# Kernel optimization log

Measured on AMD Instinct MI355X. Metric: run time of the kernel, lower is better.

The kernel has to match this reference:

```python
import jax, jax.numpy as jnp
import numpy as np

WS = 8          # window_size
WSU = 2 * WS    # window_size_up
HEADS = 8
SHIFT = WS // 2


def _build_idx(nH, nW):
    # Faithful reproduction of the torch window-reordering index (static numpy).
    if nH % 2 == 0:
        idx_H = np.arange(nH).reshape(2, -1).transpose(1, 0).reshape(-1)
    else:
        idx_H = np.arange(nH + 1).reshape(2, -1).transpose(1, 0).reshape(-1)[:-1]
    if nW % 2 == 0:
        idx_W = np.arange(nW).reshape(2, -1).transpose(1, 0).reshape(-1)
    else:
        idx_W = np.arange(nW + 1).reshape(2, -1).transpose(1, 0).reshape(-1)[:-1]
    idx = np.array([list(idx_W + i * nW) for i in range(nW)])
    return np.asarray(idx[list(idx_H)].reshape(-1))


def _rel_pos_index():
    # coords over the query window offset by ws//2; reference coords over the 2ws x 2ws KV window
    ch = np.arange(WS // 2, WS + WS // 2)
    cw = np.arange(WS // 2, WS + WS // 2)
    coords = np.stack(np.meshgrid(ch, cw, indexing='ij')).reshape(2, -1)        # (2, 64)
    rh = np.arange(2 * WS)
    rw = np.arange(2 * WS)
    ref = np.stack(np.meshgrid(rh, rw, indexing='ij')).reshape(2, -1)           # (2, 256)
    rel = coords[:, :, None] - ref[:, None, :]                                  # (2, 64, 256)
    rel = rel.transpose(1, 2, 0).copy()
    rel[..., 0] += 2 * WS - 1
    rel[..., 1] += 2 * WS - 1
    rel[..., 0] *= 4 * WS - 1
    return rel.sum(-1)  # (64, 256)


def setup_inputs() -> dict:
    key = jax.random.key(0)
    ks = jax.random.split(key, 4)
    C = 256
    return {
        'x': jax.random.normal(ks[0], (8, 128, 128, C), dtype=jnp.float32),
        'mask': jnp.zeros((1, 1, 1), dtype=jnp.float32),  # unused by the module's forward
        'qkv_w': jax.random.normal(ks[1], (3 * C, C), dtype=jnp.float32) * 0.02,
        'qkv_b': jnp.zeros((3 * C,), dtype=jnp.float32),
        'proj_w': jax.random.normal(ks[2], (C, C), dtype=jnp.float32) * 0.02,
        'proj_b': jnp.zeros((C,), dtype=jnp.float32),
        'rel_table': jax.random.normal(ks[3], ((4 * WS - 1) * (4 * WS - 1), HEADS), dtype=jnp.float32) * 0.02,
    }


def reference(x, mask, qkv_w, qkv_b, proj_w, proj_b, rel_table):
    B, H, W, C = x.shape
    hd = C // HEADS
    scale = hd ** (-0.5)

    pad_b = (WS - H % WS) % WS
    pad_r = (WS - W % WS) % WS
    x = jnp.pad(x, ((0, 0), (0, pad_b), (0, pad_r), (0, 0)))
    Hp, Wp = H + pad_b, W + pad_r

    qkv = (x @ qkv_w.T + qkv_b).reshape(B, Hp, Wp, 3, C)
    q = qkv[..., 0, :]                                    # (B, Hp, Wp, C)
    kv = jnp.moveaxis(qkv[..., 1:, :], 3, 0)              # (2, B, Hp, Wp, C)

    # pad KV for cross-window context
    kv = jnp.pad(kv, ((0, 0), (0, 0), (SHIFT, WS - SHIFT), (SHIFT, WS - SHIFT), (0, 0)))
    Hpkv, Wpkv = Hp + WS, Wp + WS

    nH, nW = Hp // WS, Wp // WS
    nHs, nWs = Hpkv // WSU, Wpkv // WSU
    nHsh, nWsh = nH - nHs, nW - nWs

    kv1 = kv[:, :, :nHs * WSU, :nWs * WSU]
    kv2 = kv[:, :, :nHs * WSU, WS:WS + nWsh * WSU]
    kv3 = kv[:, :, WS:WS + nHsh * WSU, :nWs * WSU]
    kv4 = kv[:, :, WS:WS + nHsh * WSU, WS:WS + nWsh * WSU]
    cross = jnp.concatenate([jnp.concatenate([kv1, kv2], axis=3),
                             jnp.concatenate([kv3, kv4], axis=3)], axis=2)

    # window partition at WSU -> (2, B, nH*nW, WSU*WSU, C), then reorder windows
    cross = cross.reshape(2, B, nH, WSU, nW, WSU, C).transpose(0, 1, 2, 4, 3, 5, 6)
    cross = cross.reshape(2, B, nH * nW, WSU * WSU, C)
    cross = cross[:, :, _build_idx(nH, nW)]

    Bw = B * nH * nW
    M = WSU * WSU  # 4*WS*WS KV tokens per window
    N = WS * WS    # query tokens per window
    k = cross[0].reshape(Bw, M, HEADS, hd)
    v = cross[1].reshape(Bw, M, HEADS, hd)

    qw = q.reshape(B, nH, WS, nW, WS, C).transpose(0, 1, 3, 2, 4, 5).reshape(Bw, N, HEADS, hd)

    attn = jnp.einsum('bnhd,bmhd->bhnm', qw * scale, k)   # (Bw, HEADS, N, M)
    bias = rel_table[_rel_pos_index()]                    # (N, M, HEADS)
    attn = jax.nn.softmax(attn + bias.transpose(2, 0, 1)[None], axis=-1)

    out = jnp.einsum('bhnm,bmhd->bnhd', attn, v).reshape(Bw, N, C)
    out = out @ proj_w.T + proj_b

    out = out.reshape(B, nH, nW, WS, WS, C).transpose(0, 1, 3, 2, 4, 5).reshape(B, Hp, Wp, C)
    return out[:, :H, :W, :].reshape(B, H * W, C)
```

## Files before the change

kernel.cpp:

```cpp
#include <hip/hip_runtime.h>
#include <hip/hip_bf16.h>
#include <stdint.h>

typedef __bf16 bf16;
typedef __bf16 bf16x4 __attribute__((ext_vector_type(4)));
typedef __bf16 bf16x8 __attribute__((ext_vector_type(8)));
typedef float f32x4 __attribute__((ext_vector_type(4)));

#define MFMA_BF16(a, b, c) __builtin_amdgcn_mfma_f32_16x16x32_bf16((a), (b), (c), 0, 0, 0)

#define LOG2E 1.4426950408889634f
#define QSCALE (0.17677669529663687f * 1.4426950408889634f)

__device__ __forceinline__ void load16f(const float* p, float* r) {
#pragma unroll
  for (int i = 0; i < 4; ++i) {
    float4 v = *(const float4*)(p + 4 * i);
    r[4 * i + 0] = v.x; r[4 * i + 1] = v.y; r[4 * i + 2] = v.z; r[4 * i + 3] = v.w;
  }
}

__device__ __forceinline__ void store16_bf16(bf16* dst, const float* r) {
  bf16x8 v0, v1;
#pragma unroll
  for (int i = 0; i < 8; ++i) { v0[i] = (bf16)r[i]; v1[i] = (bf16)r[8 + i]; }
  *(bf16x8*)(dst) = v0;
  *(bf16x8*)(dst + 8) = v1;
}

__global__ __launch_bounds__(256)
void cvt_bf16(const float* __restrict__ X, const float* __restrict__ Wq,
              bf16* __restrict__ Xb, bf16* __restrict__ Wqb)
{
  const unsigned t = blockIdx.x * 256 + threadIdx.x;
  const float* src;
  bf16* dst;
  if (t < 4194304u) { src = X + (size_t)t * 8; dst = Xb + (size_t)t * 8; }
  else {
    const unsigned u = t - 4194304u;
    src = Wq + (size_t)u * 8; dst = Wqb + (size_t)u * 8;
  }
  const float4 a = ((const float4*)src)[0];
  const float4 b = ((const float4*)src)[1];
  bf16x8 v;
  v[0] = (bf16)a.x; v[1] = (bf16)a.y; v[2] = (bf16)a.z; v[3] = (bf16)a.w;
  v[4] = (bf16)b.x; v[5] = (bf16)b.y; v[6] = (bf16)b.z; v[7] = (bf16)b.w;
  *(bf16x8*)dst = v;
}

__global__ void bias_pre(const float* __restrict__ rel, float* __restrict__ biasC)
{
  const int t = blockIdx.x * 256 + threadIdx.x;
  const int li = t & 15, g = (t >> 4) & 3, kt = (t >> 6) & 15;
  const int qt = (t >> 10) & 3, h = (t >> 12) & 7;
  const int n = qt * 16 + li, ni = n >> 3, nj = n & 7;
  float4 v;
  float* vp = (float*)&v;
#pragma unroll
  for (int r = 0; r < 4; ++r) {
    const int key = 32 * (kt >> 1) + 8 * g + 4 * (kt & 1) + r;
    const int ki = key >> 4, kj = key & 15;
    const int bi = (ni + 19 - ki) * 31 + (nj + 19 - kj);
    vp[r] = rel[bi * 8 + h] * LOG2E;
  }
  ((float4*)biasC)[t] = v;
}

__global__ __launch_bounds__(256, 2)
void qkv_gemm(const bf16* __restrict__ X, const bf16* __restrict__ W,
              const float* __restrict__ bias,
              bf16* __restrict__ Qb, bf16* __restrict__ Kb, bf16* __restrict__ Vg)
{
  constexpr int K = 256;
  constexpr int LD = 40;
  __shared__ bf16 As[128 * LD];
  __shared__ bf16 Bs[128 * LD];

  const int tid = threadIdx.x;
  const int lane = tid & 63, wave = tid >> 6;
  const int bid = blockIdx.x;
  const int wid = (bid & 7) * 768 + (bid >> 3);
  const int bn = wid % 6, bm = wid / 6;
  const int m0 = bm * 128, n0 = bn * 128;
  const int sr = tid >> 1, sc = (tid & 1) * 16;
  const int wr = (wave >> 1) * 64, wc = (wave & 1) * 64;
  const int g = lane >> 4, li = lane & 15;

  const f32x4 fzero = {0.f, 0.f, 0.f, 0.f};
  f32x4 acc[4][4];
#pragma unroll
  for (int i = 0; i < 4; ++i)
#pragma unroll
    for (int j = 0; j < 4; ++j) acc[i][j] = fzero;

  const bf16* Ap = X + (size_t)(m0 + sr) * K + sc;
  const bf16* Bp = W + (size_t)(n0 + sr) * K + sc;
  uint4 aV0, aV1, bV0, bV1;
  aV0 = *(const uint4*)(Ap); aV1 = *(const uint4*)(Ap + 8);
  bV0 = *(const uint4*)(Bp); bV1 = *(const uint4*)(Bp + 8);

#pragma unroll 1
  for (int kt = 0; kt < 8; ++kt) {
    *(uint4*)&As[sr * LD + sc] = aV0;
    *(uint4*)&As[sr * LD + sc + 8] = aV1;
    *(uint4*)&Bs[sr * LD + sc] = bV0;
    *(uint4*)&Bs[sr * LD + sc + 8] = bV1;
    __syncthreads();
    if (kt < 7) {
      Ap += 32; Bp += 32;
      aV0 = *(const uint4*)(Ap); aV1 = *(const uint4*)(Ap + 8);
      bV0 = *(const uint4*)(Bp); bV1 = *(const uint4*)(Bp + 8);
    }
    bf16x8 af[4], bfr[4];
#pragma unroll
    for (int t = 0; t < 4; ++t) {
      af[t]  = *(const bf16x8*)&As[(wr + t * 16 + li) * LD + g * 8];
      bfr[t] = *(const bf16x8*)&Bs[(wc + t * 16 + li) * LD + g * 8];
    }
#pragma unroll
    for (int i = 0; i < 4; ++i)
#pragma unroll
      for (int j = 0; j < 4; ++j)
        acc[i][j] = MFMA_BF16(af[i], bfr[j], acc[i][j]);
    __syncthreads();
  }

#pragma unroll
  for (int i = 0; i < 4; ++i) {
    const int row = m0 + wr + i * 16 + g * 4;
#pragma unroll
    for (int j = 0; j < 4; ++j) {
      const int col = n0 + wc + j * 16 + li;
      const float bv = bias[col];
      const int which = col >> 8;
      if (which == 2) {
        const int hh = (col >> 5) & 7, d = col & 31;
        bf16x4 pv;
#pragma unroll
        for (int r = 0; r < 4; ++r) pv[r] = (bf16)(acc[i][j][r] + bv);
        *(bf16x4*)(Vg + (((size_t)hh) << 22) + (size_t)(row >> 2) * 128 + d * 4) = pv;
      } else {
        bf16* dst = which == 0 ? Qb : Kb;
        const float sc2 = which == 0 ? QSCALE : 1.0f;
        const size_t base = (size_t)((col >> 5) & 7) * (131072u * 32u) + (size_t)(col & 31);
#pragma unroll
        for (int r = 0; r < 4; ++r)
          dst[base + (size_t)(row + r) * 32u] = (bf16)((acc[i][j][r] + bv) * sc2);
      }
    }
  }
}

__global__ __launch_bounds__(256, 4)
void win_attn(const bf16* __restrict__ Qb, const bf16* __restrict__ Kb,
              const bf16* __restrict__ Vg, const float* __restrict__ biasC,
              bf16* __restrict__ Ob)
{
  constexpr int LDK = 40;
  __shared__ bf16 Ks[256 * LDK];

  const int tid = threadIdx.x;
  const int lane = tid & 63, qt = tid >> 6;
  const int li = lane & 15, g = lane >> 4;
  const int bid = blockIdx.x;
  const int h = bid & 7, w = bid >> 3;
  const int b = w >> 8, wi = (w >> 4) & 15, wj = w & 15;
  const int btok = b << 14;

  const int q = qt * 16 + li;
  const int tokq = btok + (wi * 8 + (q >> 3)) * 128 + (wj * 8 + (q & 7));
  const bf16x8 qf = *(const bf16x8*)(Qb + ((((size_t)h) << 17) + tokq) * 32 + g * 8);

  {
    const size_t hb = ((size_t)h) << 17;
#pragma unroll
    for (int it = 0; it < 4; ++it) {
      const int u = it * 256 + tid;
      const int m = u >> 2, c = u & 3;
      const int hi = m >> 4, hj = m & 15;
      const int gi = wi * 8 - 4 + hi, gj = wj * 8 - 4 + hj;
      const bool ok = ((unsigned)gi < 128u) && ((unsigned)gj < 128u);
      uint4 kv{};
      if (ok) kv = *(const uint4*)(Kb + (hb + (size_t)(btok + gi * 128 + gj)) * 32 + c * 8);
      const int si = ((hi & 1) << 3) | ((hj >> 3) << 2) | (hj & 3);
      const int kt = ((hi >> 1) << 1) | ((hj >> 2) & 1);
      *(uint4*)&Ks[(kt * 16 + si) * LDK + c * 8] = kv;
    }
  }
  __syncthreads();

  const float* bC = biasC + (size_t)(((h * 4 + qt) * 16 * 4 + g) * 16 + li) * 4;
  f32x4 s[16];
#pragma unroll
  for (int kt = 0; kt < 16; ++kt) {
    const f32x4 c0 = *(const f32x4*)(bC + kt * 256);
    const bf16x8 kf = *(const bf16x8*)&Ks[(kt * 16 + li) * LDK + g * 8];
    s[kt] = MFMA_BF16(kf, qf, c0);
  }

  const f32x4 z4 = {0.f, 0.f, 0.f, 0.f};
  f32x4 o0 = z4, o1 = z4, o2 = z4;
  const bf16 one1 = (bf16)1.0f;
  const bf16x8 vones = {one1, one1, one1, one1, one1, one1, one1, one1};

  const int g1 = g & 1, g2 = g >> 1;
  const int gj0 = wj * 8 - 4 + 8 * g1;
  const bool c0ok = (unsigned)gj0 < 128u;
  const bool c1ok = (unsigned)(gj0 + 4) < 128u;
  const int gi0 = wi * 8 - 4 + g2;
  const bf16* vb = Vg + (((size_t)h) << 22) + (size_t)(btok >> 2) * 128 + li * 4;
  const int q4a = gj0 >> 2;

#pragma unroll
  for (int ks = 0; ks < 8; ++ks) {
    const int gi = gi0 + 2 * ks;
    const bool rok = (unsigned)gi < 128u;
    bf16x4 a0{}, a1{}, b0{}, b1{};
    if (rok & c0ok) {
      const bf16* p = vb + (size_t)(gi * 32 + q4a) * 128;
      a0 = *(const bf16x4*)p;
      b0 = *(const bf16x4*)(p + 64);
    }
    if (rok & c1ok) {
      const bf16* p = vb + (size_t)(gi * 32 + q4a + 1) * 128;
      a1 = *(const bf16x4*)p;
      b1 = *(const bf16x4*)(p + 64);
    }
    bf16x8 pb;
#pragma unroll
    for (int u = 0; u < 4; ++u) {
      pb[u]     = (bf16)exp2f(s[2 * ks][u]);
      pb[u + 4] = (bf16)exp2f(s[2 * ks + 1][u]);
    }
    const bf16x8 vf0 = __builtin_shufflevector(a0, a1, 0, 1, 2, 3, 4, 5, 6, 7);
    const bf16x8 vf1 = __builtin_shufflevector(b0, b1, 0, 1, 2, 3, 4, 5, 6, 7);
    o0 = MFMA_BF16(vf0, pb, o0);
    o1 = MFMA_BF16(vf1, pb, o1);
    o2 = MFMA_BF16(vones, pb, o2);
  }
  const float inv = __builtin_amdgcn_rcpf(o2[0]);

  bf16* op = Ob + (size_t)tokq * 256 + h * 32 + 4 * g;
  bf16x4 w0, w1;
#pragma unroll
  for (int r = 0; r < 4; ++r) {
    w0[r] = (bf16)(o0[r] * inv);
    w1[r] = (bf16)(o1[r] * inv);
  }
  *(bf16x4*)(op) = w0;
  *(bf16x4*)(op + 16) = w1;
}

__global__ __launch_bounds__(256, 2)
void proj_gemm(const bf16* __restrict__ A, const float* __restrict__ W,
               const float* __restrict__ bias, float* __restrict__ Out)
{
  constexpr int K = 256;
  constexpr int LD = 40;
  __shared__ bf16 As[128 * LD];
  __shared__ bf16 Bs[128 * LD];

  const int tid = threadIdx.x;
  const int lane = tid & 63, wave = tid >> 6;
  const int bid = blockIdx.x;
  const int wid = (bid & 7) * 256 + (bid >> 3);
  const int bn = wid & 1, bm = wid >> 1;
  const int m0 = bm * 128, n0 = bn * 128;
  const int sr = tid >> 1, sc = (tid & 1) * 16;
  const int wr = (wave >> 1) * 64, wc = (wave & 1) * 64;
  const int g = lane >> 4, li = lane & 15;

  const f32x4 fzero = {0.f, 0.f, 0.f, 0.f};
  f32x4 acc[4][4];
#pragma unroll
  for (int i = 0; i < 4; ++i)
#pragma unroll
    for (int j = 0; j < 4; ++j) acc[i][j] = fzero;

  const bf16* Ap = A + (size_t)(m0 + sr) * K + sc;
  const float* Bp = W + (size_t)(n0 + sr) * K + sc;
  uint4 aV0, aV1; float bR[16];
  aV0 = *(const uint4*)(Ap); aV1 = *(const uint4*)(Ap + 8);
  load16f(Bp, bR);

#pragma unroll 1
  for (int kt = 0; kt < 8; ++kt) {
    *(uint4*)&As[sr * LD + sc] = aV0;
    *(uint4*)&As[sr * LD + sc + 8] = aV1;
    store16_bf16(&Bs[sr * LD + sc], bR);
    __syncthreads();
    if (kt < 7) {
      Ap += 32; Bp += 32;
      aV0 = *(const uint4*)(Ap); aV1 = *(const uint4*)(Ap + 8);
      load16f(Bp, bR);
    }
    bf16x8 af[4], bfr[4];
#pragma unroll
    for (int t = 0; t < 4; ++t) {
      af[t]  = *(const bf16x8*)&As[(wr + t * 16 + li) * LD + g * 8];
      bfr[t] = *(const bf16x8*)&Bs[(wc + t * 16 + li) * LD + g * 8];
    }
#pragma unroll
    for (int i = 0; i < 4; ++i)
#pragma unroll
      for (int j = 0; j < 4; ++j)
        acc[i][j] = MFMA_BF16(af[i], bfr[j], acc[i][j]);
    __syncthreads();
  }

#pragma unroll
  for (int i = 0; i < 4; ++i) {
    const int row = m0 + wr + i * 16 + g * 4;
#pragma unroll
    for (int j = 0; j < 4; ++j) {
      const int col = n0 + wc + j * 16 + li;
      const float bv = bias[col];
#pragma unroll
      for (int r = 0; r < 4; ++r)
        Out[(size_t)(row + r) * 256 + col] = acc[i][j][r] + bv;
    }
  }
}

extern "C" void kernel_launch(void* const* d_in, const int* in_sizes, int n_in,
                              void* d_out, int out_size, void* d_ws, size_t ws_size,
                              hipStream_t stream)
{
  const float* x       = (const float*)d_in[0];
  const float* qkv_w   = (const float*)d_in[2];
  const float* qkv_b   = (const float*)d_in[3];
  const float* proj_w  = (const float*)d_in[4];
  const float* proj_b  = (const float*)d_in[5];
  const float* rel_tab = (const float*)d_in[6];
  float* out = (float*)d_out;

  char* ws = (char*)d_ws;
  bf16* Qb = (bf16*)(ws);
  bf16* Kb = (bf16*)(ws + (size_t)67108864);
  bf16* Vg = (bf16*)(ws + (size_t)134217728);
  bf16* Ao = (bf16*)(ws + (size_t)201326592);
  bf16* Xb = Ao;
  float* biasC = (float*)d_out;
  bf16*  Wqb   = (bf16*)((char*)d_out + 1048576);

  cvt_bf16<<<dim3(16480), dim3(256), 0, stream>>>(x, qkv_w, Xb, Wqb);
  bias_pre<<<dim3(128), dim3(256), 0, stream>>>(rel_tab, biasC);
  qkv_gemm<<<dim3(6144), dim3(256), 0, stream>>>(Xb, Wqb, qkv_b, Qb, Kb, Vg);
  win_attn<<<dim3(16384), dim3(256), 0, stream>>>(Qb, Kb, Vg, biasC, Ao);
  proj_gemm<<<dim3(2048), dim3(256), 0, stream>>>(Ao, proj_w, proj_b, out);
}
```

Measured before the change: 330.1 us.

## Use direct global-to-LDS loads with double buffering in QKV and projection GEMMs

Both GEMM kernels now stage A (and B for QKV) tiles through global_load_lds into double-buffered shared memory, prefetching the next k-tile while MFMAs run on the current one. This removes the register round-trip and one barrier per iteration. The cost is unpadded 32-element LDS rows, which may cause bank conflicts on fragment reads, plus doubled LDS use that can limit occupancy. The LDS layout assumes the lane-ordered placement that global_load_lds uses.

```diff
diff --git a/kernel.cpp b/kernel.cpp
--- a/kernel.cpp
+++ b/kernel.cpp
@@ -11,6 +11,11 @@
 
 #define LOG2E 1.4426950408889634f
 #define QSCALE (0.17677669529663687f * 1.4426950408889634f)
+
+#define GLL16(gp, lp)                                                          \
+  __builtin_amdgcn_global_load_lds(                                            \
+      (const __attribute__((address_space(1))) unsigned int*)(gp),             \
+      (__attribute__((address_space(3))) unsigned int*)(lp), 16, 0, 0)
 
 __device__ __forceinline__ void load16f(const float* p, float* r) {
 #pragma unroll
@@ -71,10 +76,8 @@
               const float* __restrict__ bias,
               bf16* __restrict__ Qb, bf16* __restrict__ Kb, bf16* __restrict__ Vg)
 {
-  constexpr int K = 256;
-  constexpr int LD = 40;
-  __shared__ bf16 As[128 * LD];
-  __shared__ bf16 Bs[128 * LD];
+  __shared__ bf16 As[2][128 * 32];
+  __shared__ bf16 Bs[2][128 * 32];
 
   const int tid = threadIdx.x;
   const int lane = tid & 63, wave = tid >> 6;
@@ -82,10 +85,21 @@
   const int wid = (bid & 7) * 768 + (bid >> 3);
   const int bn = wid % 6, bm = wid / 6;
   const int m0 = bm * 128, n0 = bn * 128;
-  const int sr = tid >> 1, sc = (tid & 1) * 16;
   const int wr = (wave >> 1) * 64, wc = (wave & 1) * 64;
   const int g = lane >> 4, li = lane & 15;
 
+  const bf16* agp = X + (size_t)(m0 + (tid >> 2)) * 256 + (tid & 3) * 8;
+  const bf16* bgp = W + (size_t)(n0 + (tid >> 2)) * 256 + (tid & 3) * 8;
+  const int lofs = wave * 512;
+
+#define QKV_STAGE(b, kt)                                                       \
+  do {                                                                         \
+    GLL16(agp + (kt) * 32,             &As[b][lofs]);                          \
+    GLL16(agp + (kt) * 32 + 64 * 256,  &As[b][lofs + 2048]);                   \
+    GLL16(bgp + (kt) * 32,             &Bs[b][lofs]);                          \
+    GLL16(bgp + (kt) * 32 + 64 * 256,  &Bs[b][lofs + 2048]);                   \
+  } while (0)
+
   const f32x4 fzero = {0.f, 0.f, 0.f, 0.f};
   f32x4 acc[4][4];
 #pragma unroll
@@ -93,29 +107,18 @@
 #pragma unroll
     for (int j = 0; j < 4; ++j) acc[i][j] = fzero;
 
-  const bf16* Ap = X + (size_t)(m0 + sr) * K + sc;
-  const bf16* Bp = W + (size_t)(n0 + sr) * K + sc;
-  uint4 aV0, aV1, bV0, bV1;
-  aV0 = *(const uint4*)(Ap); aV1 = *(const uint4*)(Ap + 8);
-  bV0 = *(const uint4*)(Bp); bV1 = *(const uint4*)(Bp + 8);
+  QKV_STAGE(0, 0);
+  __syncthreads();
 
 #pragma unroll 1
   for (int kt = 0; kt < 8; ++kt) {
-    *(uint4*)&As[sr * LD + sc] = aV0;
-    *(uint4*)&As[sr * LD + sc + 8] = aV1;
-    *(uint4*)&Bs[sr * LD + sc] = bV0;
-    *(uint4*)&Bs[sr * LD + sc + 8] = bV1;
-    __syncthreads();
-    if (kt < 7) {
-      Ap += 32; Bp += 32;
-      aV0 = *(const uint4*)(Ap); aV1 = *(const uint4*)(Ap + 8);
-      bV0 = *(const uint4*)(Bp); bV1 = *(const uint4*)(Bp + 8);
-    }
+    const int cur = kt & 1;
+    if (kt < 7) QKV_STAGE(cur ^ 1, kt + 1);
     bf16x8 af[4], bfr[4];
 #pragma unroll
     for (int t = 0; t < 4; ++t) {
-      af[t]  = *(const bf16x8*)&As[(wr + t * 16 + li) * LD + g * 8];
-      bfr[t] = *(const bf16x8*)&Bs[(wc + t * 16 + li) * LD + g * 8];
+      af[t]  = *(const bf16x8*)&As[cur][(wr + t * 16 + li) * 32 + g * 8];
+      bfr[t] = *(const bf16x8*)&Bs[cur][(wc + t * 16 + li) * 32 + g * 8];
     }
 #pragma unroll
     for (int i = 0; i < 4; ++i)
@@ -124,6 +127,7 @@
         acc[i][j] = MFMA_BF16(af[i], bfr[j], acc[i][j]);
     __syncthreads();
   }
+#undef QKV_STAGE
 
 #pragma unroll
   for (int i = 0; i < 4; ++i) {
@@ -255,10 +259,8 @@
 void proj_gemm(const bf16* __restrict__ A, const float* __restrict__ W,
                const float* __restrict__ bias, float* __restrict__ Out)
 {
-  constexpr int K = 256;
-  constexpr int LD = 40;
-  __shared__ bf16 As[128 * LD];
-  __shared__ bf16 Bs[128 * LD];
+  __shared__ bf16 As[2][128 * 32];
+  __shared__ bf16 Bs[2][128 * 40];
 
   const int tid = threadIdx.x;
   const int lane = tid & 63, wave = tid >> 6;
@@ -270,6 +272,10 @@
   const int wr = (wave >> 1) * 64, wc = (wave & 1) * 64;
   const int g = lane >> 4, li = lane & 15;
 
+  const bf16* agp = A + (size_t)(m0 + (tid >> 2)) * 256 + (tid & 3) * 8;
+  const float* Bp = W + (size_t)(n0 + sr) * 256 + sc;
+  const int lofs = wave * 512;
+
   const f32x4 fzero = {0.f, 0.f, 0.f, 0.f};
   f32x4 acc[4][4];
 #pragma unroll
@@ -277,28 +283,28 @@
 #pragma unroll
     for (int j = 0; j < 4; ++j) acc[i][j] = fzero;
 
-  const bf16* Ap = A + (size_t)(m0 + sr) * K + sc;
-  const float* Bp = W + (size_t)(n0 + sr) * K + sc;
-  uint4 aV0, aV1; float bR[16];
-  aV0 = *(const uint4*)(Ap); aV1 = *(const uint4*)(Ap + 8);
+  float bR[16];
   load16f(Bp, bR);
+  GLL16(agp,            &As[0][lofs]);
+  GLL16(agp + 64 * 256, &As[0][lofs + 2048]);
+  store16_bf16(&Bs[0][sr * 40 + sc], bR);
+  load16f(Bp + 32, bR);
+  __syncthreads();
 
 #pragma unroll 1
   for (int kt = 0; kt < 8; ++kt) {
-    *(uint4*)&As[sr * LD + sc] = aV0;
-    *(uint4*)&As[sr * LD + sc + 8] = aV1;
-    store16_bf16(&Bs[sr * LD + sc], bR);
-    __syncthreads();
+    const int cur = kt & 1;
     if (kt < 7) {
-      Ap += 32; Bp += 32;
-      aV0 = *(const uint4*)(Ap); aV1 = *(const uint4*)(Ap + 8);
-      load16f(Bp, bR);
+      GLL16(agp + (kt + 1) * 32,            &As[cur ^ 1][lofs]);
+      GLL16(agp + (kt + 1) * 32 + 64 * 256, &As[cur ^ 1][lofs + 2048]);
+      store16_bf16(&Bs[cur ^ 1][sr * 40 + sc], bR);
+      if (kt < 6) load16f(Bp + (kt + 2) * 32, bR);
     }
     bf16x8 af[4], bfr[4];
 #pragma unroll
     for (int t = 0; t < 4; ++t) {
-      af[t]  = *(const bf16x8*)&As[(wr + t * 16 + li) * LD + g * 8];
-      bfr[t] = *(const bf16x8*)&Bs[(wc + t * 16 + li) * LD + g * 8];
+      af[t]  = *(const bf16x8*)&As[cur][(wr + t * 16 + li) * 32 + g * 8];
+      bfr[t] = *(const bf16x8*)&Bs[cur][(wc + t * 16 + li) * 40 + g * 8];
     }
 #pragma unroll
     for (int i = 0; i < 4; ++i)
```

Result: no change. 329.6 us (-0.1%).
